# Kernel optimization log

Measured on AMD Instinct MI355X. Metric: run time of the kernel, lower is better.

## Reference

```python
import jax, jax.numpy as jnp
import numpy as np
import math

B, S, HID = 16, 1024, 1024
H, D = 16, 64  # heads, head_dim
WINDOW = 512  # pos bias length = 2*WINDOW+1 = 1025


def setup_inputs() -> dict:
    key = jax.random.key(0)
    ks = jax.random.split(key, 12)
    xav = lambda k, shp: jax.random.uniform(k, shp, jnp.float32, -1.0, 1.0) * math.sqrt(6.0 / (shp[0] + shp[1]))
    return {
        "hidden_states": jax.random.normal(ks[0], (B, S, HID), jnp.float32),
        "Wq": xav(ks[1], (HID, HID)), "bq": jnp.zeros((HID,), jnp.float32),
        "Wk": xav(ks[2], (HID, HID)), "bk": jnp.zeros((HID,), jnp.float32),
        "Wv": xav(ks[3], (HID, HID)), "bv": jnp.zeros((HID,), jnp.float32),
        "Wo": xav(ks[4], (HID, HID)), "bo": jnp.zeros((HID,), jnp.float32),
        "W_pe": xav(ks[5], (HID, 1)), "b_pe": jnp.zeros((HID,), jnp.float32),
        "pos_bias": 0.02 * jax.random.normal(ks[6], (1, H, 1, 2 * WINDOW + 1), jnp.float32),
        "clip_info": 0,
    }


def reference(hidden_states, Wq, bq, Wk, bk, Wv, bv, Wo, bo, W_pe, b_pe, pos_bias, clip_info):
    b, s, hid = hidden_states.shape
    mid = s // 2
    # relative positions in [-1, 1), shape [s, 1]
    positions = ((jnp.arange(s) - mid).astype(jnp.float32) / (mid + 1e-6))[:, None]
    pos_emb = positions @ W_pe.T + b_pe  # [s, hid]
    hs = hidden_states + pos_emb

    def heads(x):
        return x.reshape(b, s, H, D).transpose(0, 2, 1, 3)  # [b, H, s, D]

    q = heads(hs @ Wq.T + bq)
    k = heads(hs @ Wk.T + bk)
    v = heads(hs @ Wv.T + bv)

    scores = jnp.einsum("bhqd,bhkd->bhqk", q, k) / math.sqrt(D)
    scores = scores + pos_bias[:, :, :, :s]  # broadcast learned window bias over batch and query
    probs = jax.nn.softmax(scores, axis=-1)  # dropout is identity in eval mode
    ctx = jnp.einsum("bhqk,bhkd->bhqd", probs, v)
    ctx = ctx.transpose(0, 2, 1, 3).reshape(b, s, hid)
    return ctx @ Wo.T + bo
```

## Files before the change

kernel.cpp:

```cpp
#include <hip/hip_runtime.h>
#include <hip/hip_bf16.h>
#include <stdint.h>

#define BATCH 16
#define SEQ   1024
#define HIDN  1024
#define NH    16
#define HD    64
#define PBSTRIDE 1025

#define TS  64
#define AST 76

#define KSCL 0.18033688f
#define L2E  1.44269504f
#define MSUB 11.54156032f

typedef __attribute__((ext_vector_type(8))) short short8;
typedef __attribute__((ext_vector_type(4))) short short4v;
typedef __attribute__((ext_vector_type(4))) float f32x4;

__device__ __forceinline__ float bf2f(short x) {
    unsigned int u = ((unsigned int)(unsigned short)x) << 16;
    union { unsigned int u; float f; } c; c.u = u; return c.f;
}
__device__ __forceinline__ short f2bf(float f) {
    union { float f; unsigned int u; } c; c.f = f;
    unsigned int r = c.u + 0x7FFFu + ((c.u >> 16) & 1u);
    return (short)(r >> 16);
}
__device__ __forceinline__ short f2bf_fast(float f) {
    __hip_bfloat16 h = __float2bfloat16(f);
    return *reinterpret_cast<short*>(&h);
}

typedef __attribute__((address_space(1))) void gvoid;
typedef __attribute__((address_space(3))) void svoid;
__device__ __forceinline__ void gload_lds16(const void* g, void* l) {
    __builtin_amdgcn_global_load_lds((gvoid*)g, (svoid*)l, 16, 0, 0);
}

__global__ void convw4_k(const float* __restrict__ s0, const float* __restrict__ s1,
                         const float* __restrict__ s2, const float* __restrict__ s3,
                         short* __restrict__ d0, short* __restrict__ d1,
                         short* __restrict__ d2, short* __restrict__ d3) {
    const float* src = (blockIdx.y == 0) ? s0 : (blockIdx.y == 1) ? s1 : (blockIdx.y == 2) ? s2 : s3;
    short* dst       = (blockIdx.y == 0) ? d0 : (blockIdx.y == 1) ? d1 : (blockIdx.y == 2) ? d2 : d3;
    const float scl  = (blockIdx.y == 1) ? KSCL : 1.0f;
    int i = (blockIdx.x * 256 + threadIdx.x) * 4;
    float4 f = *(const float4*)(src + i);
    short4v o;
    o[0] = f2bf(f.x * scl); o[1] = f2bf(f.y * scl); o[2] = f2bf(f.z * scl); o[3] = f2bf(f.w * scl);
    *(short4v*)(dst + i) = o;
}

__global__ void convb_k(const float* __restrict__ b0, const float* __restrict__ b1,
                        const float* __restrict__ b2, float* __restrict__ fb) {
    int i = blockIdx.x * 256 + threadIdx.x;
    const float* s = (i < 1024) ? b0 : (i < 2048) ? b1 : b2;
    float scl = (i >= 1024 && i < 2048) ? KSCL : 1.0f;
    fb[i] = s[i & 1023] * scl;
}

__global__ void posemb_k(const float* __restrict__ hid, const float* __restrict__ wpe,
                         const float* __restrict__ bpe, short* __restrict__ hs) {
    long long idx = (long long)blockIdx.x * blockDim.x + threadIdx.x;
    long long base = idx * 8;
    int c = (int)(base & (HIDN - 1));
    int s = (int)((base >> 10) & (SEQ - 1));
    float pos = (float)(s - 512) * (1.0f / 512.0f);
    float4 h0 = *(const float4*)(hid + base);
    float4 h1 = *(const float4*)(hid + base + 4);
    float4 w0 = *(const float4*)(wpe + c);
    float4 w1 = *(const float4*)(wpe + c + 4);
    float4 b0 = *(const float4*)(bpe + c);
    float4 b1 = *(const float4*)(bpe + c + 4);
    short8 ov;
    ov[0] = f2bf(h0.x + pos * w0.x + b0.x);
    ov[1] = f2bf(h0.y + pos * w0.y + b0.y);
    ov[2] = f2bf(h0.z + pos * w0.z + b0.z);
    ov[3] = f2bf(h0.w + pos * w0.w + b0.w);
    ov[4] = f2bf(h1.x + pos * w1.x + b1.x);
    ov[5] = f2bf(h1.y + pos * w1.y + b1.y);
    ov[6] = f2bf(h1.z + pos * w1.z + b1.z);
    ov[7] = f2bf(h1.w + pos * w1.w + b1.w);
    *(short8*)(hs + base) = ov;
}

__global__ __launch_bounds__(256) void gemm_qkv(const short* __restrict__ A,
                                                const short* __restrict__ W,
                                                const float* __restrict__ fb,
                                                short* __restrict__ q,
                                                short* __restrict__ k,
                                                short* __restrict__ vt) {
    __shared__ __align__(16) short Als[128 * 32];
    __shared__ __align__(16) short Bls[128 * 32];
    const int tid  = threadIdx.x;
    const int lane = tid & 63;
    const int w    = tid >> 6;
    const int wr   = w >> 1, wc = w & 1;
    const int tm   = blockIdx.y * 128;
    const int tn   = blockIdx.x * 128;

    f32x4 acc[4][4] = {};

    const int srow = tid >> 2;
    const int skb  = (tid & 3) * 8;
    const long long a_base = (long long)(tm + srow) * 1024 + skb;
    const long long b_base = (long long)(tn + srow) * 1024 + skb;
    const int ldsw = w * 1024;

    const int fr = lane & 15;
    const int fg = (lane >> 4) * 8;

    for (int k0 = 0; k0 < 1024; k0 += 32) {
#pragma unroll
        for (int i = 0; i < 2; ++i) {
            gload_lds16((const void*)(A + a_base + (long long)i * 64 * 1024 + k0),
                        (void*)((char*)Als + i * 4096 + ldsw));
            gload_lds16((const void*)(W + b_base + (long long)i * 64 * 1024 + k0),
                        (void*)((char*)Bls + i * 4096 + ldsw));
        }
        __syncthreads();
        short8 af[4], bfr[4];
#pragma unroll
        for (int r = 0; r < 4; ++r) {
            af[r]  = *(const short8*)(Als + (wr * 64 + r * 16 + fr) * 32 + fg);
            bfr[r] = *(const short8*)(Bls + (wc * 64 + r * 16 + fr) * 32 + fg);
        }
#pragma unroll
        for (int mi = 0; mi < 4; ++mi)
#pragma unroll
            for (int ni = 0; ni < 4; ++ni)
                acc[mi][ni] = __builtin_amdgcn_mfma_f32_16x16x32_bf16(af[mi], bfr[ni], acc[mi][ni], 0, 0, 0);
        __syncthreads();
    }

    const int which = tn >> 10;
    short* dst = (which == 0) ? q : (which == 1) ? k : vt;
    const int g4 = (lane >> 4) * 4;
#pragma unroll
    for (int ni = 0; ni < 4; ++ni) {
        int col = tn + wc * 64 + ni * 16 + fr;
        int cc  = col & 1023;
        int h   = cc >> 6, d = cc & 63;
        float bv = fb[col];
#pragma unroll
        for (int mi = 0; mi < 4; ++mi) {
#pragma unroll
            for (int r = 0; r < 4; ++r) {
                int row = tm + wr * 64 + mi * 16 + g4 + r;
                int b = row >> 10, s = row & 1023;
                short o = f2bf(acc[mi][ni][r] + bv);
                if (which < 2)
                    dst[(((long long)(b * NH + h) * SEQ + s) << 6) + d] = o;
                else
                    dst[((long long)(b * NH + h) * HD + d) * SEQ + s] = o;
            }
        }
    }
}

__global__ __launch_bounds__(256) void gemm_out(const short* __restrict__ A,
                                                const short* __restrict__ W,
                                                const float* __restrict__ bias,
                                                float* __restrict__ Cout) {
    __shared__ __align__(16) short Als[128 * 32];
    __shared__ __align__(16) short Bls[128 * 32];
    const int tid  = threadIdx.x;
    const int lane = tid & 63;
    const int w    = tid >> 6;
    const int wr   = w >> 1, wc = w & 1;
    const int tm   = blockIdx.y * 128;
    const int tn   = blockIdx.x * 128;

    f32x4 acc[4][4] = {};

    const int srow = tid >> 2;
    const int skb  = (tid & 3) * 8;
    const long long a_base = (long long)(tm + srow) * 1024 + skb;
    const long long b_base = (long long)(tn + srow) * 1024 + skb;
    const int ldsw = w * 1024;

    const int fr = lane & 15;
    const int fg = (lane >> 4) * 8;

    for (int k0 = 0; k0 < 1024; k0 += 32) {
#pragma unroll
        for (int i = 0; i < 2; ++i) {
            gload_lds16((const void*)(A + a_base + (long long)i * 64 * 1024 + k0),
                        (void*)((char*)Als + i * 4096 + ldsw));
            gload_lds16((const void*)(W + b_base + (long long)i * 64 * 1024 + k0),
                        (void*)((char*)Bls + i * 4096 + ldsw));
        }
        __syncthreads();
        short8 af[4], bfr[4];
#pragma unroll
        for (int r = 0; r < 4; ++r) {
            af[r]  = *(const short8*)(Als + (wr * 64 + r * 16 + fr) * 32 + fg);
            bfr[r] = *(const short8*)(Bls + (wc * 64 + r * 16 + fr) * 32 + fg);
        }
#pragma unroll
        for (int mi = 0; mi < 4; ++mi)
#pragma unroll
            for (int ni = 0; ni < 4; ++ni)
                acc[mi][ni] = __builtin_amdgcn_mfma_f32_16x16x32_bf16(af[mi], bfr[ni], acc[mi][ni], 0, 0, 0);
        __syncthreads();
    }

    const int g4 = (lane >> 4) * 4;
#pragma unroll
    for (int ni = 0; ni < 4; ++ni) {
        int col = tn + wc * 64 + ni * 16 + fr;
        float bv = bias[col];
#pragma unroll
        for (int mi = 0; mi < 4; ++mi)
#pragma unroll
            for (int r = 0; r < 4; ++r) {
                int row = tm + wr * 64 + mi * 16 + g4 + r;
                Cout[(long long)row * 1024 + col] = acc[mi][ni][r] + bv;
            }
    }
}

__global__ __launch_bounds__(256) void attn_k(const short* __restrict__ Q,
                                              const short* __restrict__ Kg,
                                              const short* __restrict__ Vt,
                                              const float* __restrict__ pbias,
                                              short* __restrict__ ctx) {
    __shared__ __align__(16) short Kls[2][64 * TS];
    __shared__ __align__(16) short Vls[2][64 * TS];
    __shared__ __align__(16) short Pls[4 * 32 * AST];

    const int tid  = threadIdx.x;
    const int lane = tid & 63;
    const int w    = tid >> 6;
    const int d0   = blockIdx.x;
    const int bh   = (d0 & 7) * 32 + (d0 >> 6);
    const int qt   = (d0 >> 3) & 7;
    const int h    = bh & (NH - 1);
    const long long base = (long long)bh * (SEQ * HD);

    const int fr = lane & 15;
    const int fg = lane >> 4;

    const int trow = w * 16 + (lane >> 3);
    const int scol = ((lane & 7) ^ (lane >> 3)) * 8;
    const int ldso = w * 1024;
    const long long kg0 = base + (long long)trow * HD + scol;
    const long long vg0 = base + (long long)trow * SEQ + scol;

    short8 qf[2][2];
#pragma unroll
    for (int mi = 0; mi < 2; ++mi)
#pragma unroll
        for (int ks = 0; ks < 2; ++ks)
            qf[mi][ks] = *(const short8*)(Q + base + (long long)(qt * 128 + w * 32 + mi * 16 + fr) * HD + ks * 32 + fg * 8);

    f32x4 o[2][4] = {};
    f32x4 osum[2] = {};
    short8 vones;
#pragma unroll
    for (int j = 0; j < 8; ++j) vones[j] = (short)0x3F80;

    short* Pw = Pls + w * 32 * AST;
    const float* pbh = pbias + h * PBSTRIDE;
    const int swc = (fr & 7) << 3;

    {
        const short* ks0 = Kg + kg0;
        const short* vs0 = Vt + vg0;
        gload_lds16(ks0,           Kls[0] + ldso);
        gload_lds16(ks0 + 8 * HD,  Kls[0] + ldso + 512);
        gload_lds16(vs0,           Vls[0] + ldso);
        gload_lds16(vs0 + 8 * SEQ, Vls[0] + ldso + 512);
    }
    float pbm[4];
#pragma unroll
    for (int ni = 0; ni < 4; ++ni)
        pbm[ni] = fmaf(pbh[ni * 16 + fr], L2E, -MSUB);
    asm volatile("s_waitcnt vmcnt(0)" ::: "memory");
    __syncthreads();

    int cur = 0;
    for (int kt = 0; kt < 16; ++kt) {
        if (kt < 15) {
            const int nb = cur ^ 1;
            const short* ks0 = Kg + kg0 + (long long)((kt + 1) * 64) * HD;
            const short* vs0 = Vt + vg0 + (kt + 1) * 64;
            gload_lds16(ks0,           Kls[nb] + ldso);
            gload_lds16(ks0 + 8 * HD,  Kls[nb] + ldso + 512);
            gload_lds16(vs0,           Vls[nb] + ldso);
            gload_lds16(vs0 + 8 * SEQ, Vls[nb] + ldso + 512);
        }

        f32x4 sc[2][4];
#pragma unroll
        for (int mi = 0; mi < 2; ++mi)
#pragma unroll
            for (int ni = 0; ni < 4; ++ni)
                sc[mi][ni] = (f32x4){pbm[ni], pbm[ni], pbm[ni], pbm[ni]};
        __builtin_amdgcn_s_setprio(1);
#pragma unroll
        for (int ks = 0; ks < 2; ++ks) {
#pragma unroll
            for (int ni = 0; ni < 4; ++ni) {
                short8 kb = *(const short8*)(Kls[cur] + (ni * 16 + fr) * TS + ((ks * 32 + fg * 8) ^ swc));
#pragma unroll
                for (int mi = 0; mi < 2; ++mi)
                    sc[mi][ni] = __builtin_amdgcn_mfma_f32_16x16x32_bf16(qf[mi][ks], kb, sc[mi][ni], 0, 0, 0);
            }
        }
        __builtin_amdgcn_s_setprio(0);

#pragma unroll
        for (int mi = 0; mi < 2; ++mi)
#pragma unroll
            for (int ni = 0; ni < 4; ++ni)
#pragma unroll
                for (int r = 0; r < 4; ++r)
                    Pw[(mi * 16 + fg * 4 + r) * AST + ni * 16 + fr] =
                        f2bf_fast(exp2f(sc[mi][ni][r]));

        {
            const int nkt = (kt + 1) & 15;
#pragma unroll
            for (int ni = 0; ni < 4; ++ni)
                pbm[ni] = fmaf(pbh[nkt * 64 + ni * 16 + fr], L2E, -MSUB);
        }

        __builtin_amdgcn_s_setprio(1);
#pragma unroll
        for (int ks = 0; ks < 2; ++ks) {
            short8 pa[2];
#pragma unroll
            for (int mi = 0; mi < 2; ++mi)
                pa[mi] = *(const short8*)(Pw + (mi * 16 + fr) * AST + ks * 32 + fg * 8);
            osum[0] = __builtin_amdgcn_mfma_f32_16x16x32_bf16(pa[0], vones, osum[0], 0, 0, 0);
            osum[1] = __builtin_amdgcn_mfma_f32_16x16x32_bf16(pa[1], vones, osum[1], 0, 0, 0);
#pragma unroll
            for (int di = 0; di < 4; ++di) {
                short8 vb = *(const short8*)(Vls[cur] + (di * 16 + fr) * TS + ((ks * 32 + fg * 8) ^ swc));
#pragma unroll
                for (int mi = 0; mi < 2; ++mi)
                    o[mi][di] = __builtin_amdgcn_mfma_f32_16x16x32_bf16(pa[mi], vb, o[mi][di], 0, 0, 0);
            }
        }
        __builtin_amdgcn_s_setprio(0);

        asm volatile("s_waitcnt vmcnt(0)" ::: "memory");
        __syncthreads();
        cur ^= 1;
    }

    const int b = bh >> 4;
#pragma unroll
    for (int mi = 0; mi < 2; ++mi) {
#pragma unroll
        for (int r = 0; r < 4; ++r) {
            float inv = 1.0f / osum[mi][r];
            int srow = qt * 128 + w * 32 + mi * 16 + fg * 4 + r;
#pragma unroll
            for (int di = 0; di < 4; ++di) {
                int d = di * 16 + fr;
                ctx[(long long)(b * SEQ + srow) * HIDN + h * HD + d] = f2bf(o[mi][di][r] * inv);
            }
        }
    }
}

extern "C" void kernel_launch(void* const* d_in, const int* in_sizes, int n_in,
                              void* d_out, int out_size, void* d_ws, size_t ws_size,
                              hipStream_t stream) {
    const float* hid  = (const float*)d_in[0];
    const float* Wq   = (const float*)d_in[1];
    const float* bq   = (const float*)d_in[2];
    const float* Wk   = (const float*)d_in[3];
    const float* bk   = (const float*)d_in[4];
    const float* Wv   = (const float*)d_in[5];
    const float* bv   = (const float*)d_in[6];
    const float* Wo   = (const float*)d_in[7];
    const float* bo   = (const float*)d_in[8];
    const float* Wpe  = (const float*)d_in[9];
    const float* bpe  = (const float*)d_in[10];
    const float* pbias = (const float*)d_in[11];

    const long long NE = (long long)BATCH * SEQ * HIDN;
    const long long WSZ = (long long)HIDN * HIDN;

    short* hs   = (short*)d_ws;
    short* vt   = hs + NE;
    short* Wcq  = vt + NE;
    short* Wck  = Wcq + WSZ;
    short* Wcv  = Wck + WSZ;
    short* Wco  = Wcv + WSZ;
    float* fb   = (float*)(Wco + WSZ);
    short* q    = (short*)d_out;
    short* k    = q + NE;
    short* ctx  = hs;

    posemb_k<<<(int)(NE / 8 / 256), 256, 0, stream>>>(hid, Wpe, bpe, hs);
    convw4_k<<<dim3((int)(WSZ / 4 / 256), 4), 256, 0, stream>>>(Wq, Wk, Wv, Wo, Wcq, Wck, Wcv, Wco);
    convb_k<<<12, 256, 0, stream>>>(bq, bk, bv, fb);

    gemm_qkv<<<dim3(24, 128), 256, 0, stream>>>(hs, Wcq, fb, q, k, vt);

    attn_k<<<2048, 256, 0, stream>>>(q, k, vt, pbias, ctx);

    gemm_out<<<dim3(8, 128), 256, 0, stream>>>(ctx, Wco, bo, (float*)d_out);
}
```

Before: 397.8 us.

## Double GEMM K-step to 64 with XOR-swizzled LDS and XCD-aware tile mapping

Both GEMM kernels now stage a 64-wide K slice per iteration instead of 32, which halves the number of barrier pairs per tile. LDS rows are XOR-swizzled at 16-byte granularity to avoid bank conflicts on the wider rows. The grid is flattened to 1D and block IDs are remapped so each XCD handles a contiguous band of M rows, which should improve L2 reuse of the A operand. LDS use doubles to 32KB per block, which may lower occupancy.

```diff
diff --git a/kernel.cpp b/kernel.cpp
--- a/kernel.cpp
+++ b/kernel.cpp
@@ -93,46 +93,54 @@
                                                 short* __restrict__ q,
                                                 short* __restrict__ k,
                                                 short* __restrict__ vt) {
-    __shared__ __align__(16) short Als[128 * 32];
-    __shared__ __align__(16) short Bls[128 * 32];
+    __shared__ __align__(16) short Als[128 * 64];
+    __shared__ __align__(16) short Bls[128 * 64];
     const int tid  = threadIdx.x;
     const int lane = tid & 63;
     const int w    = tid >> 6;
     const int wr   = w >> 1, wc = w & 1;
-    const int tm   = blockIdx.y * 128;
-    const int tn   = blockIdx.x * 128;
+    const int d0   = blockIdx.x;
+    const int xcd  = d0 & 7;
+    const int idx  = d0 >> 3;
+    const int tx   = idx >> 4;
+    const int ty   = xcd * 16 + (idx & 15);
+    const int tm   = ty * 128;
+    const int tn   = tx * 128;
 
     f32x4 acc[4][4] = {};
 
-    const int srow = tid >> 2;
-    const int skb  = (tid & 3) * 8;
-    const long long a_base = (long long)(tm + srow) * 1024 + skb;
-    const long long b_base = (long long)(tn + srow) * 1024 + skb;
-    const int ldsw = w * 1024;
-
-    const int fr = lane & 15;
-    const int fg = (lane >> 4) * 8;
-
-    for (int k0 = 0; k0 < 1024; k0 += 32) {
-#pragma unroll
-        for (int i = 0; i < 2; ++i) {
-            gload_lds16((const void*)(A + a_base + (long long)i * 64 * 1024 + k0),
-                        (void*)((char*)Als + i * 4096 + ldsw));
-            gload_lds16((const void*)(W + b_base + (long long)i * 64 * 1024 + k0),
-                        (void*)((char*)Bls + i * 4096 + ldsw));
+    const int srow = w * 32 + (lane >> 3);
+    const int scol = ((lane & 7) ^ (lane >> 3)) * 8;
+    const long long a_base = (long long)(tm + srow) * 1024 + scol;
+    const long long b_base = (long long)(tn + srow) * 1024 + scol;
+    char* alds = (char*)Als + w * 4096;
+    char* blds = (char*)Bls + w * 4096;
+
+    const int fr  = lane & 15;
+    const int fg8 = (lane >> 4) * 8;
+    const int frx = (lane & 7) * 8;
+
+    for (int k0 = 0; k0 < 1024; k0 += 64) {
+#pragma unroll
+        for (int c = 0; c < 4; ++c) {
+            gload_lds16((const void*)(A + a_base + (long long)c * 8 * 1024 + k0), alds + c * 1024);
+            gload_lds16((const void*)(W + b_base + (long long)c * 8 * 1024 + k0), blds + c * 1024);
         }
         __syncthreads();
-        short8 af[4], bfr[4];
-#pragma unroll
-        for (int r = 0; r < 4; ++r) {
-            af[r]  = *(const short8*)(Als + (wr * 64 + r * 16 + fr) * 32 + fg);
-            bfr[r] = *(const short8*)(Bls + (wc * 64 + r * 16 + fr) * 32 + fg);
-        }
-#pragma unroll
-        for (int mi = 0; mi < 4; ++mi)
-#pragma unroll
-            for (int ni = 0; ni < 4; ++ni)
-                acc[mi][ni] = __builtin_amdgcn_mfma_f32_16x16x32_bf16(af[mi], bfr[ni], acc[mi][ni], 0, 0, 0);
+#pragma unroll
+        for (int ks = 0; ks < 2; ++ks) {
+            short8 af[4], bfr[4];
+#pragma unroll
+            for (int r = 0; r < 4; ++r) {
+                af[r]  = *(const short8*)(Als + (wr * 64 + r * 16 + fr) * 64 + ((ks * 32 + fg8) ^ frx));
+                bfr[r] = *(const short8*)(Bls + (wc * 64 + r * 16 + fr) * 64 + ((ks * 32 + fg8) ^ frx));
+            }
+#pragma unroll
+            for (int mi = 0; mi < 4; ++mi)
+#pragma unroll
+                for (int ni = 0; ni < 4; ++ni)
+                    acc[mi][ni] = __builtin_amdgcn_mfma_f32_16x16x32_bf16(af[mi], bfr[ni], acc[mi][ni], 0, 0, 0);
+        }
         __syncthreads();
     }
 
@@ -165,46 +173,54 @@
                                                 const short* __restrict__ W,
                                                 const float* __restrict__ bias,
                                                 float* __restrict__ Cout) {
-    __shared__ __align__(16) short Als[128 * 32];
-    __shared__ __align__(16) short Bls[128 * 32];
+    __shared__ __align__(16) short Als[128 * 64];
+    __shared__ __align__(16) short Bls[128 * 64];
     const int tid  = threadIdx.x;
     const int lane = tid & 63;
     const int w    = tid >> 6;
     const int wr   = w >> 1, wc = w & 1;
-    const int tm   = blockIdx.y * 128;
-    const int tn   = blockIdx.x * 128;
+    const int d0   = blockIdx.x;
+    const int xcd  = d0 & 7;
+    const int idx  = d0 >> 3;
+    const int tx   = idx >> 4;
+    const int ty   = xcd * 16 + (idx & 15);
+    const int tm   = ty * 128;
+    const int tn   = tx * 128;
 
     f32x4 acc[4][4] = {};
 
-    const int srow = tid >> 2;
-    const int skb  = (tid & 3) * 8;
-    const long long a_base = (long long)(tm + srow) * 1024 + skb;
-    const long long b_base = (long long)(tn + srow) * 1024 + skb;
-    const int ldsw = w * 1024;
-
-    const int fr = lane & 15;
-    const int fg = (lane >> 4) * 8;
-
-    for (int k0 = 0; k0 < 1024; k0 += 32) {
-#pragma unroll
-        for (int i = 0; i < 2; ++i) {
-            gload_lds16((const void*)(A + a_base + (long long)i * 64 * 1024 + k0),
-                        (void*)((char*)Als + i * 4096 + ldsw));
-            gload_lds16((const void*)(W + b_base + (long long)i * 64 * 1024 + k0),
-                        (void*)((char*)Bls + i * 4096 + ldsw));
+    const int srow = w * 32 + (lane >> 3);
+    const int scol = ((lane & 7) ^ (lane >> 3)) * 8;
+    const long long a_base = (long long)(tm + srow) * 1024 + scol;
+    const long long b_base = (long long)(tn + srow) * 1024 + scol;
+    char* alds = (char*)Als + w * 4096;
+    char* blds = (char*)Bls + w * 4096;
+
+    const int fr  = lane & 15;
+    const int fg8 = (lane >> 4) * 8;
+    const int frx = (lane & 7) * 8;
+
+    for (int k0 = 0; k0 < 1024; k0 += 64) {
+#pragma unroll
+        for (int c = 0; c < 4; ++c) {
+            gload_lds16((const void*)(A + a_base + (long long)c * 8 * 1024 + k0), alds + c * 1024);
+            gload_lds16((const void*)(W + b_base + (long long)c * 8 * 1024 + k0), blds + c * 1024);
         }
         __syncthreads();
-        short8 af[4], bfr[4];
-#pragma unroll
-        for (int r = 0; r < 4; ++r) {
-            af[r]  = *(const short8*)(Als + (wr * 64 + r * 16 + fr) * 32 + fg);
-            bfr[r] = *(const short8*)(Bls + (wc * 64 + r * 16 + fr) * 32 + fg);
-        }
-#pragma unroll
-        for (int mi = 0; mi < 4; ++mi)
-#pragma unroll
-            for (int ni = 0; ni < 4; ++ni)
-                acc[mi][ni] = __builtin_amdgcn_mfma_f32_16x16x32_bf16(af[mi], bfr[ni], acc[mi][ni], 0, 0, 0);
+#pragma unroll
+        for (int ks = 0; ks < 2; ++ks) {
+            short8 af[4], bfr[4];
+#pragma unroll
+            for (int r = 0; r < 4; ++r) {
+                af[r]  = *(const short8*)(Als + (wr * 64 + r * 16 + fr) * 64 + ((ks * 32 + fg8) ^ frx));
+                bfr[r] = *(const short8*)(Bls + (wc * 64 + r * 16 + fr) * 64 + ((ks * 32 + fg8) ^ frx));
+            }
+#pragma unroll
+            for (int mi = 0; mi < 4; ++mi)
+#pragma unroll
+                for (int ni = 0; ni < 4; ++ni)
+                    acc[mi][ni] = __builtin_amdgcn_mfma_f32_16x16x32_bf16(af[mi], bfr[ni], acc[mi][ni], 0, 0, 0);
+        }
         __syncthreads();
     }
 
@@ -403,9 +419,9 @@
     convw4_k<<<dim3((int)(WSZ / 4 / 256), 4), 256, 0, stream>>>(Wq, Wk, Wv, Wo, Wcq, Wck, Wcv, Wco);
     convb_k<<<12, 256, 0, stream>>>(bq, bk, bv, fb);
 
-    gemm_qkv<<<dim3(24, 128), 256, 0, stream>>>(hs, Wcq, fb, q, k, vt);
+    gemm_qkv<<<3072, 256, 0, stream>>>(hs, Wcq, fb, q, k, vt);
 
     attn_k<<<2048, 256, 0, stream>>>(q, k, vt, pbias, ctx);
 
-    gemm_out<<<dim3(8, 128), 256, 0, stream>>>(ctx, Wco, bo, (float*)d_out);
-}
+    gemm_out<<<1024, 256, 0, stream>>>(ctx, Wco, bo, (float*)d_out);
+}
```

Result: faster. 363.0 us (-8.8%).
